# Optimization experiments

Hardware: AMD Instinct MI355X
Metric: run time of the kernel (lower is better)

Reference implementation:

```python
import jax, jax.numpy as jnp
import numpy as np

N_IN = 256      # input nodes
L = 8           # layers (topological levels)
M = 4096        # nodes per layer
K = 16          # fan-in per node
B = 1024        # batch of graph evaluations
SCALE = 4.9     # config.SCALE_ACTIVATION (classic NEAT)


def setup_inputs() -> dict:
    key = jax.random.key(0)
    k1, k2, k3 = jax.random.split(key, 3)
    x = jax.random.normal(k1, (B, N_IN), dtype=jnp.float32)
    W = jax.random.normal(k2, (L, M, K), dtype=jnp.float32) * 0.3
    # edge_idx[l] must index nodes strictly before layer l:
    # valid range [0, N_IN + 1 + l*M)  (+1 is the bias node, value 1.0)
    raw = jax.random.randint(k3, (L, M, K), 0, 2**31 - 1, dtype=jnp.int32)
    offsets = (N_IN + 1 + jnp.arange(L, dtype=jnp.int32) * M)[:, None, None]
    edge_idx = raw % offsets
    return {"x": x, "W": W, "edge_idx": edge_idx}


def reference(x, W, edge_idx):
    # values buffer: inputs ++ bias node (constant 1.0) ++ layer outputs
    bias = jnp.ones((x.shape[0], 1), dtype=x.dtype)
    vals = jnp.concatenate([x, bias], axis=1)            # [B, N_IN+1]
    n_layers = W.shape[0]
    for l in range(n_layers):                            # fixed small layer count
        g = vals[:, edge_idx[l]]                         # gather: [B, M, K]
        pre = SCALE * jnp.einsum('bmk,mk->bm', g, W[l])  # per-node 1xK linear
        vals = jnp.concatenate([vals, jax.nn.sigmoid(pre)], axis=1)
    # output nodes = last layer
    return vals[:, -W.shape[1]:]                         # [B, M]
```

## Files before the change

kernel.cpp:

```cpp
#include <hip/hip_runtime.h>
#include <hip/hip_fp16.h>
#include <cstdint>

#define B_SZ   1024
#define N_IN   256
#define NLAY   8
#define M_SZ   4096
#define K_SZ   16
#define NCOLS  (N_IN + 1 + NLAY * M_SZ)
#define SCALE  4.9f
#define TPB    1024

__global__ void pack_kernel(const int* __restrict__ edge_idx,
                            const float* __restrict__ W,
                            uint32_t* __restrict__ packed, int n) {
    int i = blockIdx.x * blockDim.x + threadIdx.x;
    if (i < n) {
        uint32_t id = (uint32_t)edge_idx[i] & 0xFFFFu;
        __half h = __float2half_rn(W[i]);
        packed[i] = id | ((uint32_t)__half_as_ushort(h) << 16);
    }
}

template <bool PACKED>
__global__ __launch_bounds__(TPB, 4)
void ffn_kernel(const float* __restrict__ x,
                const uint32_t* __restrict__ packed,
                const int* __restrict__ edge_idx,
                const float* __restrict__ W,
                float* __restrict__ out) {
    __shared__ uint32_t vals[NCOLS];

    const int tid = threadIdx.x;
    const int b0  = blockIdx.x * 2;
    const float* __restrict__ x0 = x + (size_t)b0 * N_IN;
    const float* __restrict__ x1 = x0 + N_IN;

    for (int j = tid; j <= N_IN; j += TPB) {
        float v0 = (j < N_IN) ? x0[j] : 1.0f;
        float v1 = (j < N_IN) ? x1[j] : 1.0f;
        __half2 h2 = __floats2half2_rn(v0, v1);
        vals[j] = *reinterpret_cast<uint32_t*>(&h2);
    }
    __syncthreads();

    const int base = N_IN + 1;
    for (int l = 0; l < NLAY; ++l) {
        for (int i = 0; i < M_SZ / TPB; ++i) {
            const int m = tid + i * TPB;
            float acc0 = 0.f, acc1 = 0.f;

            if (PACKED) {
                const uint4* p4 =
                    reinterpret_cast<const uint4*>(packed + (size_t)(l * M_SZ + m) * K_SZ);
                uint4 pw[4];
                #pragma unroll
                for (int j = 0; j < 4; ++j) pw[j] = p4[j];
                #pragma unroll
                for (int j = 0; j < 4; ++j) {
                    uint32_t w0 = pw[j].x, w1 = pw[j].y, w2 = pw[j].z, w3 = pw[j].w;
                    uint32_t words[4] = {w0, w1, w2, w3};
                    #pragma unroll
                    for (int q = 0; q < 4; ++q) {
                        uint32_t p = words[q];
                        uint32_t v = vals[p & 0xFFFFu];
                        float wf = __half2float(__ushort_as_half((unsigned short)(p >> 16)));
                        __half2 h2 = *reinterpret_cast<__half2*>(&v);
                        acc0 = fmaf(__low2float(h2), wf, acc0);
                        acc1 = fmaf(__high2float(h2), wf, acc1);
                    }
                }
            } else {
                const int4*   i4 = reinterpret_cast<const int4*>(edge_idx + (size_t)(l * M_SZ + m) * K_SZ);
                const float4* w4 = reinterpret_cast<const float4*>(W + (size_t)(l * M_SZ + m) * K_SZ);
                #pragma unroll
                for (int j = 0; j < 4; ++j) {
                    int4   ii = i4[j];
                    float4 ww = w4[j];
                    int   idxs[4] = {ii.x, ii.y, ii.z, ii.w};
                    float wts[4]  = {ww.x, ww.y, ww.z, ww.w};
                    #pragma unroll
                    for (int q = 0; q < 4; ++q) {
                        uint32_t v = vals[idxs[q]];
                        __half2 h2 = *reinterpret_cast<__half2*>(&v);
                        acc0 = fmaf(__low2float(h2), wts[q], acc0);
                        acc1 = fmaf(__high2float(h2), wts[q], acc1);
                    }
                }
            }

            float s0 = 1.0f / (1.0f + __expf(-SCALE * acc0));
            float s1 = 1.0f / (1.0f + __expf(-SCALE * acc1));

            if (l < NLAY - 1) {
                __half2 h2 = __floats2half2_rn(s0, s1);
                vals[base + l * M_SZ + m] = *reinterpret_cast<uint32_t*>(&h2);
            } else {
                out[(size_t)b0 * M_SZ + m]       = s0;
                out[(size_t)(b0 + 1) * M_SZ + m] = s1;
            }
        }
        __syncthreads();
    }
}

extern "C" void kernel_launch(void* const* d_in, const int* in_sizes, int n_in,
                              void* d_out, int out_size, void* d_ws, size_t ws_size,
                              hipStream_t stream) {
    const float* x        = (const float*)d_in[0];
    const float* W        = (const float*)d_in[1];
    const int*   edge_idx = (const int*)d_in[2];
    float*       out      = (float*)d_out;

    const int n = NLAY * M_SZ * K_SZ;
    if (ws_size >= (size_t)n * sizeof(uint32_t)) {
        uint32_t* packed = (uint32_t*)d_ws;
        pack_kernel<<<(n + 255) / 256, 256, 0, stream>>>(edge_idx, W, packed, n);
        ffn_kernel<true><<<B_SZ / 2, TPB, 0, stream>>>(x, packed, nullptr, nullptr, out);
    } else {
        ffn_kernel<false><<<B_SZ / 2, TPB, 0, stream>>>(x, nullptr, edge_idx, W, out);
    }
}
```

Measured before the change: 77.39 us.

## Reorder per-node edges to balance LDS bank conflicts across wave lanes

Replaces the simple pack kernel with a scheduling pack kernel. For each wave of 64 nodes it greedily assigns each of a node's 16 edges to a slot, using per-slot, per-bank load counters in shared memory so that lanes reading the same slot hit different LDS banks. Because the sum over edges is order-independent, the main kernel's gathers from the shared value buffer should see fewer bank conflicts. The cost is a serial greedy loop with LDS atomics in the pre-pass, which runs on far fewer blocks than before.

```diff
diff --git a/kernel.cpp b/kernel.cpp
--- a/kernel.cpp
+++ b/kernel.cpp
@@ -11,14 +11,56 @@
 #define SCALE  4.9f
 #define TPB    1024
 
-__global__ void pack_kernel(const int* __restrict__ edge_idx,
-                            const float* __restrict__ W,
-                            uint32_t* __restrict__ packed, int n) {
-    int i = blockIdx.x * blockDim.x + threadIdx.x;
-    if (i < n) {
-        uint32_t id = (uint32_t)edge_idx[i] & 0xFFFFu;
-        __half h = __float2half_rn(W[i]);
-        packed[i] = id | ((uint32_t)__half_as_ushort(h) << 16);
+__global__ __launch_bounds__(256)
+void sched_pack_kernel(const int* __restrict__ edge_idx,
+                       const float* __restrict__ W,
+                       uint32_t* __restrict__ packed) {
+    __shared__ uint32_t load[4][16][32];
+
+    const int wave = threadIdx.x >> 6;
+    const int lane = threadIdx.x & 63;
+    const int g    = blockIdx.x * 4 + wave;
+    const int l    = g >> 6;
+    const int mblk = g & 63;
+    const int m    = mblk * 64 + lane;
+    const int base = (l * M_SZ + m) * K_SZ;
+
+    int   idxv[16];
+    float wv[16];
+    const int4*   ip = reinterpret_cast<const int4*>(edge_idx + base);
+    const float4* wp = reinterpret_cast<const float4*>(W + base);
+    #pragma unroll
+    for (int j = 0; j < 4; ++j) {
+        int4   ii = ip[j];
+        float4 ww = wp[j];
+        idxv[4*j+0] = ii.x; idxv[4*j+1] = ii.y; idxv[4*j+2] = ii.z; idxv[4*j+3] = ii.w;
+        wv[4*j+0]   = ww.x; wv[4*j+1]   = ww.y; wv[4*j+2]   = ww.z; wv[4*j+3]   = ww.w;
+    }
+
+    uint32_t* lw = &load[wave][0][0];
+    #pragma unroll
+    for (int s = 0; s < 8; ++s) lw[lane + s * 64] = 0;
+    __syncthreads();
+
+    uint32_t amask = 0;
+    for (int r = 0; r < 16; ++r) {
+        const int b = idxv[r] & 31;
+        uint32_t bestload = 0xFFFFFFFFu;
+        int      best     = 0;
+        #pragma unroll
+        for (int s = 0; s < 16; ++s) {
+            uint32_t ld = load[wave][s][b];
+            ld = (amask & (1u << s)) ? 0xFFFFFFFFu : ld;
+            if (ld < bestload) { bestload = ld; best = s; }
+        }
+        amask |= 1u << best;
+        __builtin_amdgcn_sched_barrier(0);
+        atomicAdd(&load[wave][best][b], 1u);
+        __builtin_amdgcn_sched_barrier(0);
+
+        uint32_t p = ((uint32_t)idxv[r] & 0xFFFFu) |
+                     ((uint32_t)__half_as_ushort(__float2half_rn(wv[r])) << 16);
+        packed[base + best] = p;
     }
 }
 
@@ -58,8 +100,7 @@
                 for (int j = 0; j < 4; ++j) pw[j] = p4[j];
                 #pragma unroll
                 for (int j = 0; j < 4; ++j) {
-                    uint32_t w0 = pw[j].x, w1 = pw[j].y, w2 = pw[j].z, w3 = pw[j].w;
-                    uint32_t words[4] = {w0, w1, w2, w3};
+                    uint32_t words[4] = {pw[j].x, pw[j].y, pw[j].z, pw[j].w};
                     #pragma unroll
                     for (int q = 0; q < 4; ++q) {
                         uint32_t p = words[q];
@@ -115,7 +156,7 @@
     const int n = NLAY * M_SZ * K_SZ;
     if (ws_size >= (size_t)n * sizeof(uint32_t)) {
         uint32_t* packed = (uint32_t*)d_ws;
-        pack_kernel<<<(n + 255) / 256, 256, 0, stream>>>(edge_idx, W, packed, n);
+        sched_pack_kernel<<<128, 256, 0, stream>>>(edge_idx, W, packed);
         ffn_kernel<true><<<B_SZ / 2, TPB, 0, stream>>>(x, packed, nullptr, nullptr, out);
     } else {
         ffn_kernel<false><<<B_SZ / 2, TPB, 0, stream>>>(x, nullptr, edge_idx, W, out);
```

New measurement: 81.15 us. +4.9%, slower.
